# Performance work log

Hardware: AMD Instinct MI355X
Metric: run time of the kernel (lower is better)

Reference implementation:

```python
import jax, jax.numpy as jnp
import numpy as np

B = 1024      # num graphs
NPG = 128     # nodes per graph
N = B * NPG
EPG = 512     # edges per graph
E = B * EPG
D = 64
MAX_STEPS = 4
S = MAX_STEPS + 1   # max_steps + stop-step offset
T = 1.0
TB = 1.0
NEG = -1e30
STOP = -1


def setup_inputs() -> dict:
    key = jax.random.key(0)
    ks = jax.random.split(key, 24)
    edge_batch = jnp.repeat(jnp.arange(B, dtype=jnp.int32), EPG)
    src = jax.random.randint(ks[0], (E,), 0, NPG, dtype=jnp.int32) + edge_batch * NPG
    dst = jax.random.randint(ks[1], (E,), 0, NPG, dtype=jnp.int32) + edge_batch * NPG
    edge_index = jnp.stack([src, dst])
    sc = 1.0 / np.sqrt(D)
    p = lambda k, shape: (jax.random.normal(k, shape, jnp.float32) * sc)
    return dict(
        node_tokens=p(ks[2], (N, D)), edge_emb=p(ks[3], (E, D)),
        Wf1=p(ks[4], (D, D)), Wnf=p(ks[5], (D, D)), Wf2=p(ks[6], (D, D)),
        bf=jnp.zeros((D,), jnp.float32), wf=p(ks[7], (D,)),
        Wb1=p(ks[8], (D, D)), Wnb=p(ks[9], (D, D)), Wb2=p(ks[10], (D, D)),
        bb=jnp.zeros((D,), jnp.float32), wb=p(ks[11], (D,)),
        w_stop=p(ks[12], (D,)), b_stop=jnp.zeros((), jnp.float32),
        Ws=p(ks[13], (D, D)), Wu=p(ks[14], (D, D)), bu=jnp.zeros((D,), jnp.float32),
        edge_index=edge_index, edge_batch=edge_batch,
    )


def reference(node_tokens, edge_emb, Wf1, Wnf, Wf2, bf, wf,
              Wb1, Wnb, Wb2, bb, wb, w_stop, b_stop, Ws, Wu, bu,
              edge_index, edge_batch):
    esrc, edst = edge_index[0], edge_index[1]
    # state-independent part of the edge scores (precomputed once; faithful math)
    base_f = edge_emb @ Wf1 + node_tokens[esrc] @ Wnf + bf   # [E,D]
    base_b = edge_emb @ Wb1 + node_tokens[edst] @ Wnb + bb   # [E,D]
    g_ids = jnp.arange(B, dtype=jnp.int32)
    eidx = jnp.arange(E, dtype=jnp.int32)

    def seg_lse(x, valid):
        # per-graph logsumexp over valid edges (grad-safe masking)
        xm = jnp.where(valid, x, NEG)
        m = jax.ops.segment_max(xm, edge_batch, num_segments=B)
        xc = jnp.where(valid, x - m[edge_batch], 0.0)
        s = jax.ops.segment_sum(jnp.where(valid, jnp.exp(xc), 0.0), edge_batch, num_segments=B)
        return m + jnp.log(jnp.maximum(s, 1e-30))

    def step_fn(carry, k):
        state_vec, active, used, done, steps, stopn = carry
        valid = (esrc == active[edge_batch]) & (~used) & (~done[edge_batch])
        allow_stop = (~done) & (steps < MAX_STEPS)
        # forward edge scores + stop logit
        h = jax.nn.relu(base_f + (state_vec @ Wf2)[edge_batch])   # [E,D]
        score = h @ wf                                            # [E]
        stop_logit = state_vec @ w_stop + b_stop                  # [B]
        x = score / T
        lse_e = seg_lse(x, valid)
        stop_t = jnp.where(allow_stop, stop_logit / T, NEG)
        Z = jnp.logaddexp(lse_e, stop_t)
        logp_edge = x - Z[edge_batch]
        logp_stop = jnp.where(allow_stop, stop_logit / T - Z, 0.0)
        has_edge = jax.ops.segment_sum(valid.astype(jnp.int32), edge_batch, num_segments=B) > 0
        # gumbel-max sampling with scatter_max semantics
        ke, ksn = jax.random.split(k)
        se = jnp.where(valid, logp_edge + jax.random.gumbel(ke, (E,)), NEG)
        ss = jnp.where(allow_stop, logp_stop + jax.random.gumbel(ksn, (B,)), NEG)
        m = jax.ops.segment_max(se, edge_batch, num_segments=B)
        amax = jax.ops.segment_min(jnp.where(se == m[edge_batch], eidx, E), edge_batch, num_segments=B)
        amax = jnp.where(has_edge, amax, 0).astype(jnp.int32)
        m = jnp.where(has_edge, m, NEG)
        choose_stop = (ss > m) | (~has_edge)
        actions = jnp.where(choose_stop | done, STOP, amax)
        log_pf = jnp.where(choose_stop, logp_stop, logp_edge[amax])
        log_pf = jnp.where(done, 0.0, log_pf)
        take_edge = (actions >= 0) & (~done)
        stopping = choose_stop & (~done)
        stopn = jnp.where((stopn < 0) & stopping, active - g_ids * NPG, stopn)
        # state encoder update (masked)
        rel = edge_emb[amax]                                      # [B,D]
        new_state = jnp.tanh(state_vec @ Ws + rel @ Wu + bu)
        state_vec = jnp.where(take_edge[:, None], new_state, state_vec)
        # env step
        new_active = jnp.where(take_edge, edst[amax], active)
        used = used.at[amax].max(take_edge)
        steps = steps + take_edge.astype(jnp.int32)
        new_done = done | stopping
        # backward policy log-prob over edges incoming to the new active node
        bvalid = edst == new_active[edge_batch]
        hb = jax.nn.relu(base_b + (state_vec @ Wb2)[edge_batch])
        xb = (hb @ wb) / TB
        lse_b = seg_lse(xb, bvalid)
        log_pb = jnp.where(take_edge, xb[amax] - lse_b, 0.0)
        return (state_vec, new_active, used, new_done, steps, stopn), (actions, log_pf, log_pb)

    init = (
        jnp.zeros((B, D), jnp.float32),      # state_vec
        g_ids * NPG,                          # active node (global) = graph start node
        jnp.zeros((E,), bool),                # used_edge_mask
        jnp.zeros((B,), bool),                # done
        jnp.zeros((B,), jnp.int32),           # step_counts
        jnp.full((B,), STOP, jnp.int32),      # stop_node_locals
    )
    keys = jax.random.split(jax.random.key(42), S)
    (state_vec, active, used, done, steps, stopn), ys = jax.lax.scan(step_fn, init, keys)
    actions_seq = ys[0].T      # [B,S]
    log_pf_steps = ys[1].T     # [B,S]
    log_pb_steps = ys[2].T     # [B,S]
    stopn = jnp.where(stopn < 0, active - g_ids * NPG, stopn)   # backfill stop nodes
    return (actions_seq, log_pf_steps.sum(1), log_pf_steps, log_pb_steps,
            used, stopn, steps.astype(jnp.float32))
```

## Files before the change

kernel.cpp:

```cpp
#include <hip/hip_runtime.h>
#include <hip/hip_bf16.h>
#include <cstdint>

#define NBLK 1024
#define NPG  128
#define EPG  512
#define DD   64
#define NSTEP 5
#define ETOT (NBLK*EPG)
#define NEGF (-1e30f)
#define WAVES 4
#define MAXDEG 32

#define OA  0
#define OLS 5120
#define OPF 6144
#define OPB 11264
#define OU  16384
#define OSN 540672
#define OST 541696

struct KeysArg {
  uint32_t ke0[NSTEP], ke1[NSTEP];
  uint32_t ks0[NSTEP], ks1[NSTEP];
};

__host__ __device__ inline uint32_t rotl32(uint32_t x, int r){ return (x<<r)|(x>>(32-r)); }

__host__ __device__ inline void tf2x32(uint32_t k0, uint32_t k1, uint32_t& x0, uint32_t& x1){
  uint32_t k2 = k0 ^ k1 ^ 0x1BD11BDAu;
  x0 += k0; x1 += k1;
  x0+=x1; x1=rotl32(x1,13); x1^=x0;
  x0+=x1; x1=rotl32(x1,15); x1^=x0;
  x0+=x1; x1=rotl32(x1,26); x1^=x0;
  x0+=x1; x1=rotl32(x1, 6); x1^=x0;
  x0+=k1; x1+=k2+1u;
  x0+=x1; x1=rotl32(x1,17); x1^=x0;
  x0+=x1; x1=rotl32(x1,29); x1^=x0;
  x0+=x1; x1=rotl32(x1,16); x1^=x0;
  x0+=x1; x1=rotl32(x1,24); x1^=x0;
  x0+=k2; x1+=k0+2u;
  x0+=x1; x1=rotl32(x1,13); x1^=x0;
  x0+=x1; x1=rotl32(x1,15); x1^=x0;
  x0+=x1; x1=rotl32(x1,26); x1^=x0;
  x0+=x1; x1=rotl32(x1, 6); x1^=x0;
  x0+=k0; x1+=k1+3u;
  x0+=x1; x1=rotl32(x1,17); x1^=x0;
  x0+=x1; x1=rotl32(x1,29); x1^=x0;
  x0+=x1; x1=rotl32(x1,16); x1^=x0;
  x0+=x1; x1=rotl32(x1,24); x1^=x0;
  x0+=k1; x1+=k2+4u;
  x0+=x1; x1=rotl32(x1,13); x1^=x0;
  x0+=x1; x1=rotl32(x1,15); x1^=x0;
  x0+=x1; x1=rotl32(x1,26); x1^=x0;
  x0+=x1; x1=rotl32(x1, 6); x1^=x0;
  x0+=k2; x1+=k0+5u;
}

__device__ inline float gumbel_from_bits(uint32_t bits){
  float f = __uint_as_float((bits>>9) | 0x3f800000u) - 1.0f;
  const float tiny = 1.17549435e-38f;
  float u = fmaxf(tiny, f * (1.0f - tiny) + tiny);
  return -logf(-logf(u));
}

__device__ inline float gumbel_part(uint32_t k0, uint32_t k1, uint32_t idx){
  uint32_t x0 = 0u, x1 = idx;
  tf2x32(k0, k1, x0, x1);
  return gumbel_from_bits(x0 ^ x1);
}

__device__ inline float wsum(float x){
  #pragma unroll
  for (int off = 32; off; off >>= 1) x += __shfl_xor(x, off, 64);
  return x;
}

__device__ __forceinline__ float rdlane(float v, int i){
  return __int_as_float(__builtin_amdgcn_readlane(__float_as_int(v), i));
}

__device__ __forceinline__ float matvec_col(const float* __restrict__ W, float v, int lane){
  float a0=0.f, a1=0.f, a2=0.f, a3=0.f;
  #pragma unroll 4
  for (int i = 0; i < DD; i += 4){
    a0 = fmaf(rdlane(v, i  ), W[(i  )*DD+lane], a0);
    a1 = fmaf(rdlane(v, i+1), W[(i+1)*DD+lane], a1);
    a2 = fmaf(rdlane(v, i+2), W[(i+2)*DD+lane], a2);
    a3 = fmaf(rdlane(v, i+3), W[(i+3)*DD+lane], a3);
  }
  return (a0+a1)+(a2+a3);
}

__device__ __forceinline__ void matvec4(const float* __restrict__ W,
                                        float v0, float v1, float v2, float v3,
                                        int lane, float o[4]){
  float acc[4][4] = {{0,0,0,0},{0,0,0,0},{0,0,0,0},{0,0,0,0}};
  #pragma unroll 4
  for (int i = 0; i < DD; i += 4){
    #pragma unroll
    for (int t = 0; t < 4; t++){
      float w  = W[(i+t)*DD+lane];
      acc[0][t] = fmaf(rdlane(v0, i+t), w, acc[0][t]);
      acc[1][t] = fmaf(rdlane(v1, i+t), w, acc[1][t]);
      acc[2][t] = fmaf(rdlane(v2, i+t), w, acc[2][t]);
      acc[3][t] = fmaf(rdlane(v3, i+t), w, acc[3][t]);
    }
  }
  #pragma unroll
  for (int c = 0; c < 4; c++)
    o[c] = (acc[c][0]+acc[c][1])+(acc[c][2]+acc[c][3]);
}

__global__ void __launch_bounds__(256)
gfn_fused(const float* __restrict__ node_tokens,
          const float* __restrict__ edge_emb,
          const float* __restrict__ Wf1, const float* __restrict__ Wnf, const float* __restrict__ Wf2,
          const float* __restrict__ bf,  const float* __restrict__ wf,
          const float* __restrict__ Wb1, const float* __restrict__ Wnb, const float* __restrict__ Wb2,
          const float* __restrict__ bb,  const float* __restrict__ wb,
          const float* __restrict__ w_stop, const float* __restrict__ b_stop,
          const float* __restrict__ Ws,  const float* __restrict__ Wu, const float* __restrict__ bu,
          const int* __restrict__ e_src, const int* __restrict__ e_dst,
          float* __restrict__ out, KeysArg keys)
{
  const int g    = blockIdx.x;
  const int tid  = threadIdx.x;
  const int lane = tid & 63;
  const int wave = tid >> 6;
  const int ebase = g * EPG;

  __shared__ uint8_t  srcL[EPG], dstL[EPG];
  __shared__ uint16_t listO[EPG], listI[EPG];
  __shared__ int cntO[NPG], cntI[NPG], begO[NPG], begI[NPG];
  __shared__ uint8_t usedL[EPG];
  __shared__ float st[DD];
  __shared__ float a_sh[MAXDEG][DD];
  __shared__ float u_sh[DD], nt_sh[DD];
  __shared__ float ub_sh[DD], ntb_sh[DD];
  __shared__ float acs_sh[DD], acr_sh[DD];
  __shared__ float xc[MAXDEG], gm[MAXDEG];
  __shared__ float sl_sh, gs_sh, sh_xbb;

  for (int j = tid; j < EPG; j += 256){
    srcL[j] = (uint8_t)(e_src[ebase+j] - g*NPG);
    dstL[j] = (uint8_t)(e_dst[ebase+j] - g*NPG);
    usedL[j] = 0;
  }
  for (int n = tid; n < NPG; n += 256){ cntO[n]=0; cntI[n]=0; }
  if (tid < DD) st[tid] = 0.f;
  __syncthreads();

  for (int j = tid; j < EPG; j += 256){
    atomicAdd(&cntO[srcL[j]], 1);
    atomicAdd(&cntI[dstL[j]], 1);
  }
  __syncthreads();

  if (wave == 0){
    int n0 = lane*2, n1 = n0+1;
    int c0O=cntO[n0], c1O=cntO[n1], sO=c0O+c1O;
    int c0I=cntI[n0], c1I=cntI[n1], sI=c0I+c1I;
    int xO=sO, xI=sI;
    #pragma unroll
    for (int off=1; off<64; off<<=1){
      int tO=__shfl_up(xO,off,64), tI=__shfl_up(xI,off,64);
      if (lane>=off){ xO+=tO; xI+=tI; }
    }
    begO[n0]=xO-sO; begO[n1]=xO-c1O;
    begI[n0]=xI-sI; begI[n1]=xI-c1I;
  }
  __syncthreads();
  for (int n = tid; n < NPG; n += 256){ cntO[n]=0; cntI[n]=0; }
  __syncthreads();

  for (int ph = 0; ph < WAVES; ph++){
    if (wave == ph){
      #pragma unroll
      for (int h = 0; h < 2; h++){
        int j = ph*128 + h*64 + lane;
        int sL = srcL[j]; int p = atomicAdd(&cntO[sL],1); listO[begO[sL]+p] = (uint16_t)j;
        int dL = dstL[j]; int q = atomicAdd(&cntI[dL],1); listI[begI[dL]+q] = (uint16_t)j;
      }
    }
    __syncthreads();
  }

  const float bf_l = bf[lane], wf_l = wf[lane];
  const float bb_l = bb[lane], wb_l = wb[lane];
  const float wst_l = w_stop[lane];
  const float bstop = b_stop[0];

  bool done = false;
  int stepsC = 0;
  int stopn = -1;
  int activeL = 0;
  float lpf_sum = 0.f;

  for (int s = 0; s < NSTEP; s++){
    float act_out = -1.f, lpf_out = 0.f, lpb_out = 0.f;
    if (!done){
      const int bO = begO[activeL];
      const int dOc = min(cntO[activeL], MAXDEG);
      float st_v = st[lane];

      if (wave == 0){
        u_sh[lane] = matvec_col(Wf2, st_v, lane);
      } else if (wave == 1){
        float ntv = node_tokens[(size_t)(g*NPG + activeL)*DD + lane];
        nt_sh[lane] = matvec_col(Wnf, ntv, lane);
      } else if (wave == 2){
        for (int base = 0; base < dOc; base += 4){
          float v[4];
          #pragma unroll
          for (int t = 0; t < 4; t++){
            int k = base + t;
            int el = listO[bO + min(k, dOc-1)];
            v[t] = edge_emb[(size_t)(ebase+el)*DD + lane];
          }
          float o[4];
          matvec4(Wf1, v[0], v[1], v[2], v[3], lane, o);
          #pragma unroll
          for (int t = 0; t < 4; t++){
            int k = base + t;
            if (k < dOc) a_sh[k][lane] = o[t];
          }
        }
      } else {
        float sl = wsum(st_v * wst_l) + bstop;
        if (lane == 0) sl_sh = sl;
        if (lane < dOc){
          int el = listO[bO + lane];
          gm[lane] = gumbel_part(keys.ke0[s], keys.ke1[s], (uint32_t)(ebase+el));
        }
        if (lane == 63) gs_sh = gumbel_part(keys.ks0[s], keys.ks1[s], (uint32_t)g);
      }
      __syncthreads();

      for (int k = wave; k < dOc; k += WAVES){
        int el = listO[bO + k];
        float x = NEGF;
        if (!usedL[el]){
          float h = fmaxf(a_sh[k][lane] + nt_sh[lane] + bf_l + u_sh[lane], 0.f);
          x = wsum(h * wf_l);
        }
        if (lane == 0) xc[k] = x;
      }
      __syncthreads();

      float sl = sl_sh;
      float m1 = NEGF; int nvalid = 0;
      for (int k=0;k<dOc;k++){ float xk=xc[k]; if (xk!=NEGF){ m1=fmaxf(m1,xk); nvalid++; } }
      float ssum = 0.f;
      for (int k=0;k<dOc;k++){ float xk=xc[k]; if (xk!=NEGF) ssum += expf(xk - m1); }
      const bool has_edge = nvalid > 0;
      float lse_e = m1 + logf(fmaxf(ssum, 1e-30f));
      const bool allow_stop = (stepsC < 4);
      float stop_t = allow_stop ? sl : NEGF;
      float amx = fmaxf(lse_e, stop_t);
      float Z = amx + log1pf(expf(-fabsf(lse_e - stop_t)));

      float mbest = NEGF; int elbest = -1; float xbest = 0.f;
      for (int k=0;k<dOc;k++){
        float xk = xc[k];
        if (xk == NEGF) continue;
        float se = (xk - Z) + gm[k];
        if (se > mbest){ mbest = se; elbest = listO[bO+k]; xbest = xk; }
      }
      float ss = allow_stop ? (sl - Z) + gs_sh : NEGF;
      float mcmp = has_edge ? mbest : NEGF;
      const bool choose_stop = (ss > mcmp) || (!has_edge);
      float logp_stop = allow_stop ? (sl - Z) : 0.f;
      const bool take_edge = !choose_stop;

      act_out = choose_stop ? -1.f : (float)(ebase + elbest);
      lpf_out = choose_stop ? logp_stop : (xbest - Z);
      if (choose_stop && stopn < 0) stopn = activeL;

      if (take_edge){
        if (wave == 0){
          acs_sh[lane] = matvec_col(Ws, st_v, lane);
        } else if (wave == 1){
          float rv = edge_emb[(size_t)(ebase+elbest)*DD + lane];
          acr_sh[lane] = matvec_col(Wu, rv, lane);
        }
      }
      __syncthreads();
      if (take_edge){
        if (tid < DD) st[tid] = tanhf(acs_sh[tid] + acr_sh[tid] + bu[tid]);
        if (tid == 0) usedL[elbest] = 1;
        activeL = dstL[elbest];
        stepsC++;
      }
      __syncthreads();

      const int bI = begI[activeL];
      const int dIc = take_edge ? min(cntI[activeL], MAXDEG) : 0;
      if (take_edge){
        if (wave == 0){
          ub_sh[lane] = matvec_col(Wb2, st[lane], lane);
        } else if (wave == 1){
          float nbv = node_tokens[(size_t)(g*NPG + activeL)*DD + lane];
          ntb_sh[lane] = matvec_col(Wnb, nbv, lane);
        } else if (wave == 2){
          for (int base = 0; base < dIc; base += 4){
            float v[4];
            #pragma unroll
            for (int t = 0; t < 4; t++){
              int k = base + t;
              int el = listI[bI + min(k, dIc-1)];
              v[t] = edge_emb[(size_t)(ebase+el)*DD + lane];
            }
            float o[4];
            matvec4(Wb1, v[0], v[1], v[2], v[3], lane, o);
            #pragma unroll
            for (int t = 0; t < 4; t++){
              int k = base + t;
              if (k < dIc) a_sh[k][lane] = o[t];
            }
          }
        }
      }
      __syncthreads();

      if (take_edge){
        for (int k = wave; k < dIc; k += WAVES){
          int el = listI[bI + k];
          float h = fmaxf(a_sh[k][lane] + ntb_sh[lane] + bb_l + ub_sh[lane], 0.f);
          float xb = wsum(h * wb_l);
          if (lane == 0){ xc[k] = xb; if (el == elbest) sh_xbb = xb; }
        }
      }
      __syncthreads();
      if (take_edge){
        float m2 = NEGF;
        for (int k=0;k<dIc;k++) m2 = fmaxf(m2, xc[k]);
        float s2 = 0.f;
        for (int k=0;k<dIc;k++) s2 += expf(xc[k] - m2);
        float lse_b = m2 + logf(fmaxf(s2, 1e-30f));
        lpb_out = sh_xbb - lse_b;
      }
      done = done || choose_stop;
      __syncthreads();
    }

    if (tid == 0){
      out[OA  + g*NSTEP + s] = act_out;
      out[OPF + g*NSTEP + s] = lpf_out;
      out[OPB + g*NSTEP + s] = lpb_out;
    }
    lpf_sum += lpf_out;
  }

  if (tid == 0){
    out[OLS + g] = lpf_sum;
    int sn = (stopn < 0) ? activeL : stopn;
    out[OSN + g] = (float)sn;
    out[OST + g] = (float)stepsC;
  }
  for (int j = tid; j < EPG; j += 256)
    out[OU + ebase + j] = usedL[j] ? 1.0f : 0.0f;
}

extern "C" void kernel_launch(void* const* d_in, const int* in_sizes, int n_in,
                              void* d_out, int out_size, void* d_ws, size_t ws_size,
                              hipStream_t stream)
{
  (void)in_sizes; (void)n_in; (void)out_size; (void)d_ws; (void)ws_size;

  KeysArg K;
  for (uint32_t s = 0; s < NSTEP; s++){
    uint32_t a = 0u, b = s;
    tf2x32(0u, 42u, a, b);
    uint32_t e0 = 0u, e1 = 0u;
    tf2x32(a, b, e0, e1);
    uint32_t s0 = 0u, s1 = 1u;
    tf2x32(a, b, s0, s1);
    K.ke0[s] = e0; K.ke1[s] = e1;
    K.ks0[s] = s0; K.ks1[s] = s1;
  }

  const int* eidx = (const int*)d_in[17];
  gfn_fused<<<dim3(NBLK), dim3(256), 0, stream>>>(
      (const float*)d_in[0],  (const float*)d_in[1],
      (const float*)d_in[2],  (const float*)d_in[3],  (const float*)d_in[4],
      (const float*)d_in[5],  (const float*)d_in[6],
      (const float*)d_in[7],  (const float*)d_in[8],  (const float*)d_in[9],
      (const float*)d_in[10], (const float*)d_in[11],
      (const float*)d_in[12], (const float*)d_in[13],
      (const float*)d_in[14], (const float*)d_in[15], (const float*)d_in[16],
      eidx, eidx + ETOT,
      (float*)d_out, K);
}
```

Measured before the change: 91.91 us.

## Collapse per-graph block to a single wavefront, removing barriers and shared staging

Each graph now runs on one 64-lane wavefront instead of four. The work that was split across waves (matvecs, edge projection, gumbel sampling) runs serially in that one wave, and paired matvecs are interleaved. State and intermediate vectors stay in registers, so the shared-memory staging and every __syncthreads are gone. The change trades intra-graph parallelism for lower sync and LDS overhead and smaller blocks that may allow more resident blocks. It risks a longer serial critical path per graph, with 1024 blocks on a large GPU.

```diff
diff --git a/kernel.cpp b/kernel.cpp
--- a/kernel.cpp
+++ b/kernel.cpp
@@ -9,7 +9,6 @@
 #define NSTEP 5
 #define ETOT (NBLK*EPG)
 #define NEGF (-1e30f)
-#define WAVES 4
 #define MAXDEG 32
 
 #define OA  0
@@ -92,6 +91,25 @@
   return (a0+a1)+(a2+a3);
 }
 
+__device__ __forceinline__ void matvec_col2(const float* __restrict__ Wa, float va,
+                                            const float* __restrict__ Wb, float vb,
+                                            int lane, float& oa, float& ob){
+  float a0=0.f,a1=0.f,a2=0.f,a3=0.f, b0=0.f,b1=0.f,b2=0.f,b3=0.f;
+  #pragma unroll 4
+  for (int i = 0; i < DD; i += 4){
+    a0 = fmaf(rdlane(va, i  ), Wa[(i  )*DD+lane], a0);
+    b0 = fmaf(rdlane(vb, i  ), Wb[(i  )*DD+lane], b0);
+    a1 = fmaf(rdlane(va, i+1), Wa[(i+1)*DD+lane], a1);
+    b1 = fmaf(rdlane(vb, i+1), Wb[(i+1)*DD+lane], b1);
+    a2 = fmaf(rdlane(va, i+2), Wa[(i+2)*DD+lane], a2);
+    b2 = fmaf(rdlane(vb, i+2), Wb[(i+2)*DD+lane], b2);
+    a3 = fmaf(rdlane(va, i+3), Wa[(i+3)*DD+lane], a3);
+    b3 = fmaf(rdlane(vb, i+3), Wb[(i+3)*DD+lane], b3);
+  }
+  oa = (a0+a1)+(a2+a3);
+  ob = (b0+b1)+(b2+b3);
+}
+
 __device__ __forceinline__ void matvec4(const float* __restrict__ W,
                                         float v0, float v1, float v2, float v3,
                                         int lane, float o[4]){
@@ -112,7 +130,7 @@
     o[c] = (acc[c][0]+acc[c][1])+(acc[c][2]+acc[c][3]);
 }
 
-__global__ void __launch_bounds__(256)
+__global__ void __launch_bounds__(64)
 gfn_fused(const float* __restrict__ node_tokens,
           const float* __restrict__ edge_emb,
           const float* __restrict__ Wf1, const float* __restrict__ Wnf, const float* __restrict__ Wf2,
@@ -125,39 +143,32 @@
           float* __restrict__ out, KeysArg keys)
 {
   const int g    = blockIdx.x;
-  const int tid  = threadIdx.x;
-  const int lane = tid & 63;
-  const int wave = tid >> 6;
+  const int lane = threadIdx.x;
   const int ebase = g * EPG;
 
   __shared__ uint8_t  srcL[EPG], dstL[EPG];
   __shared__ uint16_t listO[EPG], listI[EPG];
   __shared__ int cntO[NPG], cntI[NPG], begO[NPG], begI[NPG];
   __shared__ uint8_t usedL[EPG];
-  __shared__ float st[DD];
-  __shared__ float a_sh[MAXDEG][DD];
-  __shared__ float u_sh[DD], nt_sh[DD];
-  __shared__ float ub_sh[DD], ntb_sh[DD];
-  __shared__ float acs_sh[DD], acr_sh[DD];
   __shared__ float xc[MAXDEG], gm[MAXDEG];
-  __shared__ float sl_sh, gs_sh, sh_xbb;
-
-  for (int j = tid; j < EPG; j += 256){
+
+  #pragma unroll
+  for (int r = 0; r < 8; r++){
+    int j = r*64 + lane;
     srcL[j] = (uint8_t)(e_src[ebase+j] - g*NPG);
     dstL[j] = (uint8_t)(e_dst[ebase+j] - g*NPG);
     usedL[j] = 0;
   }
-  for (int n = tid; n < NPG; n += 256){ cntO[n]=0; cntI[n]=0; }
-  if (tid < DD) st[tid] = 0.f;
-  __syncthreads();
-
-  for (int j = tid; j < EPG; j += 256){
+  cntO[lane]=0; cntO[lane+64]=0; cntI[lane]=0; cntI[lane+64]=0;
+
+  #pragma unroll
+  for (int r = 0; r < 8; r++){
+    int j = r*64 + lane;
     atomicAdd(&cntO[srcL[j]], 1);
     atomicAdd(&cntI[dstL[j]], 1);
   }
-  __syncthreads();
-
-  if (wave == 0){
+
+  {
     int n0 = lane*2, n1 = n0+1;
     int c0O=cntO[n0], c1O=cntO[n1], sO=c0O+c1O;
     int c0I=cntI[n0], c1I=cntI[n1], sI=c0I+c1I;
@@ -170,27 +181,21 @@
     begO[n0]=xO-sO; begO[n1]=xO-c1O;
     begI[n0]=xI-sI; begI[n1]=xI-c1I;
   }
-  __syncthreads();
-  for (int n = tid; n < NPG; n += 256){ cntO[n]=0; cntI[n]=0; }
-  __syncthreads();
-
-  for (int ph = 0; ph < WAVES; ph++){
-    if (wave == ph){
-      #pragma unroll
-      for (int h = 0; h < 2; h++){
-        int j = ph*128 + h*64 + lane;
-        int sL = srcL[j]; int p = atomicAdd(&cntO[sL],1); listO[begO[sL]+p] = (uint16_t)j;
-        int dL = dstL[j]; int q = atomicAdd(&cntI[dL],1); listI[begI[dL]+q] = (uint16_t)j;
-      }
-    }
-    __syncthreads();
+  cntO[lane]=0; cntO[lane+64]=0; cntI[lane]=0; cntI[lane+64]=0;
+
+  #pragma unroll
+  for (int r = 0; r < 8; r++){
+    int j = r*64 + lane;
+    int sL = srcL[j]; int p = atomicAdd(&cntO[sL],1); listO[begO[sL]+p] = (uint16_t)j;
+    int dL = dstL[j]; int q = atomicAdd(&cntI[dL],1); listI[begI[dL]+q] = (uint16_t)j;
   }
 
   const float bf_l = bf[lane], wf_l = wf[lane];
   const float bb_l = bb[lane], wb_l = wb[lane];
-  const float wst_l = w_stop[lane];
+  const float bu_l = bu[lane], wst_l = w_stop[lane];
   const float bstop = b_stop[0];
 
+  float st_v = 0.f;
   bool done = false;
   int stepsC = 0;
   int stopn = -1;
@@ -202,53 +207,42 @@
     if (!done){
       const int bO = begO[activeL];
       const int dOc = min(cntO[activeL], MAXDEG);
-      float st_v = st[lane];
-
-      if (wave == 0){
-        u_sh[lane] = matvec_col(Wf2, st_v, lane);
-      } else if (wave == 1){
-        float ntv = node_tokens[(size_t)(g*NPG + activeL)*DD + lane];
-        nt_sh[lane] = matvec_col(Wnf, ntv, lane);
-      } else if (wave == 2){
-        for (int base = 0; base < dOc; base += 4){
-          float v[4];
-          #pragma unroll
-          for (int t = 0; t < 4; t++){
-            int k = base + t;
-            int el = listO[bO + min(k, dOc-1)];
-            v[t] = edge_emb[(size_t)(ebase+el)*DD + lane];
-          }
-          float o[4];
-          matvec4(Wf1, v[0], v[1], v[2], v[3], lane, o);
-          #pragma unroll
-          for (int t = 0; t < 4; t++){
-            int k = base + t;
-            if (k < dOc) a_sh[k][lane] = o[t];
+
+      float ntv = node_tokens[(size_t)(g*NPG + activeL)*DD + lane];
+      float u_j, nt_j;
+      matvec_col2(Wf2, st_v, Wnf, ntv, lane, u_j, nt_j);
+      float sl = wsum(st_v * wst_l) + bstop;
+
+      if (lane < dOc){
+        int el = listO[bO + lane];
+        gm[lane] = gumbel_part(keys.ke0[s], keys.ke1[s], (uint32_t)(ebase+el));
+      }
+      float gs = gumbel_part(keys.ks0[s], keys.ks1[s], (uint32_t)g);
+
+      for (int base = 0; base < dOc; base += 4){
+        int el[4]; float v[4];
+        #pragma unroll
+        for (int t = 0; t < 4; t++){
+          int k = base + t;
+          el[t] = listO[bO + min(k, dOc-1)];
+          v[t]  = edge_emb[(size_t)(ebase+el[t])*DD + lane];
+        }
+        float o[4];
+        matvec4(Wf1, v[0], v[1], v[2], v[3], lane, o);
+        #pragma unroll
+        for (int t = 0; t < 4; t++){
+          int k = base + t;
+          if (k < dOc){
+            float x = NEGF;
+            if (!usedL[el[t]]){
+              float h = fmaxf(o[t] + nt_j + bf_l + u_j, 0.f);
+              x = wsum(h * wf_l);
+            }
+            if (lane == 0) xc[k] = x;
           }
         }
-      } else {
-        float sl = wsum(st_v * wst_l) + bstop;
-        if (lane == 0) sl_sh = sl;
-        if (lane < dOc){
-          int el = listO[bO + lane];
-          gm[lane] = gumbel_part(keys.ke0[s], keys.ke1[s], (uint32_t)(ebase+el));
-        }
-        if (lane == 63) gs_sh = gumbel_part(keys.ks0[s], keys.ks1[s], (uint32_t)g);
       }
-      __syncthreads();
-
-      for (int k = wave; k < dOc; k += WAVES){
-        int el = listO[bO + k];
-        float x = NEGF;
-        if (!usedL[el]){
-          float h = fmaxf(a_sh[k][lane] + nt_sh[lane] + bf_l + u_sh[lane], 0.f);
-          x = wsum(h * wf_l);
-        }
-        if (lane == 0) xc[k] = x;
-      }
-      __syncthreads();
-
-      float sl = sl_sh;
+
       float m1 = NEGF; int nvalid = 0;
       for (int k=0;k<dOc;k++){ float xk=xc[k]; if (xk!=NEGF){ m1=fmaxf(m1,xk); nvalid++; } }
       float ssum = 0.f;
@@ -267,7 +261,7 @@
         float se = (xk - Z) + gm[k];
         if (se > mbest){ mbest = se; elbest = listO[bO+k]; xbest = xk; }
       }
-      float ss = allow_stop ? (sl - Z) + gs_sh : NEGF;
+      float ss = allow_stop ? (sl - Z) + gs : NEGF;
       float mcmp = has_edge ? mbest : NEGF;
       const bool choose_stop = (ss > mcmp) || (!has_edge);
       float logp_stop = allow_stop ? (sl - Z) : 0.f;
@@ -278,73 +272,53 @@
       if (choose_stop && stopn < 0) stopn = activeL;
 
       if (take_edge){
-        if (wave == 0){
-          acs_sh[lane] = matvec_col(Ws, st_v, lane);
-        } else if (wave == 1){
-          float rv = edge_emb[(size_t)(ebase+elbest)*DD + lane];
-          acr_sh[lane] = matvec_col(Wu, rv, lane);
-        }
-      }
-      __syncthreads();
-      if (take_edge){
-        if (tid < DD) st[tid] = tanhf(acs_sh[tid] + acr_sh[tid] + bu[tid]);
-        if (tid == 0) usedL[elbest] = 1;
+        float rv = edge_emb[(size_t)(ebase+elbest)*DD + lane];
+        float acs, acr;
+        matvec_col2(Ws, st_v, Wu, rv, lane, acs, acr);
+        st_v = tanhf(acs + acr + bu_l);
+        if (lane == 0) usedL[elbest] = 1;
         activeL = dstL[elbest];
         stepsC++;
-      }
-      __syncthreads();
-
-      const int bI = begI[activeL];
-      const int dIc = take_edge ? min(cntI[activeL], MAXDEG) : 0;
-      if (take_edge){
-        if (wave == 0){
-          ub_sh[lane] = matvec_col(Wb2, st[lane], lane);
-        } else if (wave == 1){
-          float nbv = node_tokens[(size_t)(g*NPG + activeL)*DD + lane];
-          ntb_sh[lane] = matvec_col(Wnb, nbv, lane);
-        } else if (wave == 2){
-          for (int base = 0; base < dIc; base += 4){
-            float v[4];
-            #pragma unroll
-            for (int t = 0; t < 4; t++){
-              int k = base + t;
-              int el = listI[bI + min(k, dIc-1)];
-              v[t] = edge_emb[(size_t)(ebase+el)*DD + lane];
-            }
-            float o[4];
-            matvec4(Wb1, v[0], v[1], v[2], v[3], lane, o);
-            #pragma unroll
-            for (int t = 0; t < 4; t++){
-              int k = base + t;
-              if (k < dIc) a_sh[k][lane] = o[t];
+
+        float nbv = node_tokens[(size_t)(g*NPG + activeL)*DD + lane];
+        float ntb_j, ub_j;
+        matvec_col2(Wnb, nbv, Wb2, st_v, lane, ntb_j, ub_j);
+
+        const int bI = begI[activeL];
+        const int dIc = min(cntI[activeL], MAXDEG);
+        float xbb = 0.f;
+        for (int base = 0; base < dIc; base += 4){
+          int el[4]; float v[4];
+          #pragma unroll
+          for (int t = 0; t < 4; t++){
+            int k = base + t;
+            el[t] = listI[bI + min(k, dIc-1)];
+            v[t]  = edge_emb[(size_t)(ebase+el[t])*DD + lane];
+          }
+          float o[4];
+          matvec4(Wb1, v[0], v[1], v[2], v[3], lane, o);
+          #pragma unroll
+          for (int t = 0; t < 4; t++){
+            int k = base + t;
+            if (k < dIc){
+              float h = fmaxf(o[t] + ntb_j + bb_l + ub_j, 0.f);
+              float xb = wsum(h * wb_l);
+              if (lane == 0) xc[k] = xb;
+              if (el[t] == elbest) xbb = xb;
             }
           }
         }
-      }
-      __syncthreads();
-
-      if (take_edge){
-        for (int k = wave; k < dIc; k += WAVES){
-          int el = listI[bI + k];
-          float h = fmaxf(a_sh[k][lane] + ntb_sh[lane] + bb_l + ub_sh[lane], 0.f);
-          float xb = wsum(h * wb_l);
-          if (lane == 0){ xc[k] = xb; if (el == elbest) sh_xbb = xb; }
-        }
-      }
-      __syncthreads();
-      if (take_edge){
         float m2 = NEGF;
         for (int k=0;k<dIc;k++) m2 = fmaxf(m2, xc[k]);
         float s2 = 0.f;
         for (int k=0;k<dIc;k++) s2 += expf(xc[k] - m2);
         float lse_b = m2 + logf(fmaxf(s2, 1e-30f));
-        lpb_out = sh_xbb - lse_b;
+        lpb_out = xbb - lse_b;
       }
       done = done || choose_stop;
-      __syncthreads();
     }
 
-    if (tid == 0){
+    if (lane == 0){
       out[OA  + g*NSTEP + s] = act_out;
       out[OPF + g*NSTEP + s] = lpf_out;
       out[OPB + g*NSTEP + s] = lpb_out;
@@ -352,14 +326,17 @@
     lpf_sum += lpf_out;
   }
 
-  if (tid == 0){
+  if (lane == 0){
     out[OLS + g] = lpf_sum;
     int sn = (stopn < 0) ? activeL : stopn;
     out[OSN + g] = (float)sn;
     out[OST + g] = (float)stepsC;
   }
-  for (int j = tid; j < EPG; j += 256)
+  #pragma unroll
+  for (int r = 0; r < 8; r++){
+    int j = r*64 + lane;
     out[OU + ebase + j] = usedL[j] ? 1.0f : 0.0f;
+  }
 }
 
 extern "C" void kernel_launch(void* const* d_in, const int* in_sizes, int n_in,
@@ -381,7 +358,7 @@
   }
 
   const int* eidx = (const int*)d_in[17];
-  gfn_fused<<<dim3(NBLK), dim3(256), 0, stream>>>(
+  gfn_fused<<<dim3(NBLK), dim3(64), 0, stream>>>(
       (const float*)d_in[0],  (const float*)d_in[1],
       (const float*)d_in[2],  (const float*)d_in[3],  (const float*)d_in[4],
       (const float*)d_in[5],  (const float*)d_in[6],
```

Measured after the change: 96.53 us. 5.0% more time.
